# Performance work log

Hardware: AMD Instinct MI355X
Metric: run time of the kernel (lower is better)

Reference implementation:

```python
import jax, jax.numpy as jnp
import numpy as np

HEADS = 8
D = 1024


def setup_inputs() -> dict:
    key = jax.random.key(0)
    ks = jax.random.split(key, 10)
    B, Sq, Sk = 8, 2048, 2048
    x = jax.random.normal(ks[0], (B, Sq, D), dtype=jnp.float32)
    context = jax.random.normal(ks[1], (B, Sk, D), dtype=jnp.float32)
    # Dense params (glorot-ish scale)
    def dense(k, fin, fout):
        return jax.random.normal(k, (fin, fout), dtype=jnp.float32) / np.sqrt(fin)
    Wq = dense(ks[2], D, HEADS); bq = jnp.zeros((HEADS,), jnp.float32)
    Wk = dense(ks[3], D, HEADS); bk = jnp.zeros((HEADS,), jnp.float32)
    Wv = dense(ks[4], D, HEADS); bv = jnp.zeros((HEADS,), jnp.float32)
    Wo = dense(ks[5], HEADS, D); bo = jnp.zeros((D,), jnp.float32)
    return {"x": x, "context": context, "Wq": Wq, "bq": bq,
            "Wk": Wk, "bk": bk, "Wv": Wv, "bv": bv, "Wo": Wo, "bo": bo}


def reference(x, context, Wq, bq, Wk, bk, Wv, bv, Wo, bo):
    # q: [B,Sq,H], k/v: [B,Sk,H]  (H = heads = projection width, no head split)
    q = jnp.einsum('bsd,dh->bsh', x, Wq) + bq
    k = jnp.einsum('btd,dh->bth', context, Wk) + bk
    v = jnp.einsum('btd,dh->bth', context, Wv) + bv
    # Dot(axes=-1): scores[b,s,t] = q[b,s,:] . k[b,t,:]  -> [B,Sq,Sk]
    scores = jnp.einsum('bsh,bth->bst', q, k)
    weights = jax.nn.softmax(scores, axis=-1)  # no 1/sqrt(d) scaling in original
    # Dot(axes=(-1,1)): out[b,s,h] = sum_t weights[b,s,t] * v[b,t,h]
    out = jnp.einsum('bst,bth->bsh', weights, v)
    return jnp.einsum('bsh,hd->bsd', out, Wo) + bo
```

## Files before the change

### kernel.cpp

```cpp
#include <hip/hip_runtime.h>

constexpr int D = 1024;
constexpr int H = 8;
constexpr int S = 2048;
constexpr int B = 8;
constexpr int NROW = B * S;

__device__ __forceinline__ int swz(int i) { return i ^ ((i >> 3) & 7); }

__global__ __launch_bounds__(256)
void proj_kernel(const float* __restrict__ x, const float* __restrict__ ctx,
                 const float* __restrict__ Wq, const float* __restrict__ bq,
                 const float* __restrict__ Wk, const float* __restrict__ bk,
                 const float* __restrict__ Wv, const float* __restrict__ bv,
                 float* __restrict__ qo, float* __restrict__ ko,
                 float* __restrict__ vo)
{
    __shared__ float4 wlds[2048];
    const int tid = threadIdx.x;
    const int tensor = (int)blockIdx.x % 3;
    const int blk    = (int)blockIdx.x / 3;

    const float* W    = (tensor == 0) ? Wq : (tensor == 1) ? Wk : Wv;
    const float* bias = (tensor == 0) ? bq : (tensor == 1) ? bk : bv;
    const float* src  = (tensor == 0) ? x  : ctx;
    float*       dst  = (tensor == 0) ? qo : (tensor == 1) ? ko : vo;

    {
        const float4* w4 = (const float4*)W;
        for (int i = tid; i < 2048; i += 256) wlds[swz(i)] = w4[i];
    }
    __syncthreads();

    const int c    = tid & 15;
    const int team = tid >> 4;
    const int row0 = blk * 64 + team * 4;
    const float4* r0 = (const float4*)(src + (size_t)row0 * D);

    float4 a0[4], a1[4];
#pragma unroll
    for (int r = 0; r < 4; ++r) {
        a0[r] = make_float4(0.f, 0.f, 0.f, 0.f);
        a1[r] = make_float4(0.f, 0.f, 0.f, 0.f);
    }

#pragma unroll 2
    for (int j = 0; j < 16; ++j) {
        float4 xv[4];
#pragma unroll
        for (int r = 0; r < 4; ++r) xv[r] = r0[r * 256 + 16 * j + c];
        const int ib = 128 * j + 8 * c;
#pragma unroll
        for (int e = 0; e < 4; ++e) {
            const float4 w0 = wlds[swz(ib + 2 * e)];
            const float4 w1 = wlds[swz(ib + 2 * e + 1)];
#pragma unroll
            for (int r = 0; r < 4; ++r) {
                const float s = (&xv[r].x)[e];
                a0[r].x += s * w0.x; a0[r].y += s * w0.y;
                a0[r].z += s * w0.z; a0[r].w += s * w0.w;
                a1[r].x += s * w1.x; a1[r].y += s * w1.y;
                a1[r].z += s * w1.z; a1[r].w += s * w1.w;
            }
        }
    }

#pragma unroll
    for (int r = 0; r < 4; ++r) {
        float s[8] = {a0[r].x, a0[r].y, a0[r].z, a0[r].w,
                      a1[r].x, a1[r].y, a1[r].z, a1[r].w};
#pragma unroll
        for (int h = 0; h < 8; ++h) {
            s[h] += __shfl_down(s[h], 8);
            s[h] += __shfl_down(s[h], 4);
            s[h] += __shfl_down(s[h], 2);
            s[h] += __shfl_down(s[h], 1);
        }
        if (c == 0) {
            float4* o = (float4*)(dst + (size_t)(row0 + r) * H);
            o[0] = make_float4(s[0] + bias[0], s[1] + bias[1],
                               s[2] + bias[2], s[3] + bias[3]);
            o[1] = make_float4(s[4] + bias[4], s[5] + bias[5],
                               s[6] + bias[6], s[7] + bias[7]);
        }
    }
}

constexpr int ROWS_PER_WAVE = 4;
constexpr int ROWS_PER_BLOCK = 16;
constexpr int TILE_T = 512;

__global__ __launch_bounds__(256)
void attn_kernel(const float* __restrict__ q, const float* __restrict__ k,
                 const float* __restrict__ v, const float* __restrict__ Wo,
                 const float* __restrict__ bo, float* __restrict__ out)
{
    __shared__ float4 kt[TILE_T * 2];
    __shared__ float4 vt[TILE_T * 2];
    const int tid  = threadIdx.x;
    const int lane = tid & 63;
    const int wid  = tid >> 6;

    const int row0 = blockIdx.x * ROWS_PER_BLOCK + wid * ROWS_PER_WAVE;
    const int b = row0 >> 11;

    float qv[ROWS_PER_WAVE][H];
#pragma unroll
    for (int r = 0; r < ROWS_PER_WAVE; ++r) {
        const float4* q4 = (const float4*)(q + (size_t)(row0 + r) * H);
        const float4 a = q4[0], c = q4[1];
        qv[r][0] = a.x; qv[r][1] = a.y; qv[r][2] = a.z; qv[r][3] = a.w;
        qv[r][4] = c.x; qv[r][5] = c.y; qv[r][6] = c.z; qv[r][7] = c.w;
    }

    float l[ROWS_PER_WAVE] = {0.f, 0.f, 0.f, 0.f};
    float o[ROWS_PER_WAVE][H];
#pragma unroll
    for (int r = 0; r < ROWS_PER_WAVE; ++r)
#pragma unroll
        for (int h = 0; h < H; ++h) o[r][h] = 0.f;

    const float4* kg = (const float4*)(k + (size_t)b * S * H);
    const float4* vg = (const float4*)(v + (size_t)b * S * H);

    for (int tile = 0; tile < S / TILE_T; ++tile) {
        __syncthreads();
#pragma unroll
        for (int i = 0; i < 4; ++i) {
            kt[i * 256 + tid] = kg[tile * 1024 + i * 256 + tid];
            vt[i * 256 + tid] = vg[tile * 1024 + i * 256 + tid];
        }
        __syncthreads();
#pragma unroll 2
        for (int m = 0; m < TILE_T / 64; ++m) {
            const int t2 = (lane + (m << 6)) * 2;
            const float4 ka = kt[t2], kb = kt[t2 + 1];
            const float4 va = vt[t2], vb = vt[t2 + 1];
#pragma unroll
            for (int r = 0; r < ROWS_PER_WAVE; ++r) {
                const float s = qv[r][0] * ka.x + qv[r][1] * ka.y
                              + qv[r][2] * ka.z + qv[r][3] * ka.w
                              + qv[r][4] * kb.x + qv[r][5] * kb.y
                              + qv[r][6] * kb.z + qv[r][7] * kb.w;
                const float e = __expf(s);
                l[r] += e;
                o[r][0] += e * va.x; o[r][1] += e * va.y;
                o[r][2] += e * va.z; o[r][3] += e * va.w;
                o[r][4] += e * vb.x; o[r][5] += e * vb.y;
                o[r][6] += e * vb.z; o[r][7] += e * vb.w;
            }
        }
    }

#pragma unroll
    for (int r = 0; r < ROWS_PER_WAVE; ++r) {
#pragma unroll
        for (int off = 32; off > 0; off >>= 1) l[r] += __shfl_xor(l[r], off);
        const float inv = 1.f / l[r];
#pragma unroll
        for (int h = 0; h < H; ++h) {
#pragma unroll
            for (int off = 32; off > 0; off >>= 1) o[r][h] += __shfl_xor(o[r][h], off);
            o[r][h] *= inv;
        }
    }

    const float4* Wo4 = (const float4*)Wo;
    const float4* bo4 = (const float4*)bo;
    float4* out4 = (float4*)out;
#pragma unroll
    for (int c = 0; c < 4; ++c) {
        const int f = lane + 64 * c;
        float4 w[H];
#pragma unroll
        for (int h = 0; h < H; ++h) w[h] = Wo4[h * (D / 4) + f];
        const float4 base = bo4[f];
#pragma unroll
        for (int r = 0; r < ROWS_PER_WAVE; ++r) {
            float4 acc = base;
#pragma unroll
            for (int h = 0; h < H; ++h) {
                acc.x += o[r][h] * w[h].x;
                acc.y += o[r][h] * w[h].y;
                acc.z += o[r][h] * w[h].z;
                acc.w += o[r][h] * w[h].w;
            }
            out4[(size_t)(row0 + r) * (D / 4) + f] = acc;
        }
    }
}

extern "C" void kernel_launch(void* const* d_in, const int* in_sizes, int n_in,
                              void* d_out, int out_size, void* d_ws, size_t ws_size,
                              hipStream_t stream) {
    const float* x   = (const float*)d_in[0];
    const float* ctx = (const float*)d_in[1];
    const float* Wq  = (const float*)d_in[2];
    const float* bq  = (const float*)d_in[3];
    const float* Wk  = (const float*)d_in[4];
    const float* bk  = (const float*)d_in[5];
    const float* Wv  = (const float*)d_in[6];
    const float* bv  = (const float*)d_in[7];
    const float* Wo  = (const float*)d_in[8];
    const float* bo  = (const float*)d_in[9];
    float* out = (float*)d_out;

    float* qw = (float*)d_ws;
    float* kw = qw + (size_t)NROW * H;
    float* vw = kw + (size_t)NROW * H;

    proj_kernel<<<dim3(3 * NROW / 64), dim3(256), 0, stream>>>(
        x, ctx, Wq, bq, Wk, bk, Wv, bv, qw, kw, vw);
    attn_kernel<<<dim3(NROW / ROWS_PER_BLOCK), dim3(256), 0, stream>>>(
        qw, kw, vw, Wo, bo, out);
}
```

Baseline: 238.1 us.

## Prefetch x rows in projection, split K/V LDS tiles, double rows per wave

The projection kernel now keeps four register buffers of input rows and issues loads four steps ahead, so global-load latency overlaps the FMA work. The attention kernel doubles the query rows per wave (4→8, block 16→32 rows), reusing each K/V tile read from LDS across more rows and halving the number of times K/V are staged. K/V are also split into separate low/high float4 LDS arrays to avoid strided 32-byte LDS accesses. The cost is more registers per thread, which may lower occupancy, and half as many attention blocks.

```diff
diff --git a/kernel.cpp b/kernel.cpp
--- a/kernel.cpp
+++ b/kernel.cpp
@@ -44,11 +44,20 @@
         a1[r] = make_float4(0.f, 0.f, 0.f, 0.f);
     }
 
-#pragma unroll 2
-    for (int j = 0; j < 16; ++j) {
-        float4 xv[4];
-#pragma unroll
-        for (int r = 0; r < 4; ++r) xv[r] = r0[r * 256 + 16 * j + c];
+    float4 bA[4], bB[4], bC[4], bD[4];
+#pragma unroll
+    for (int r = 0; r < 4; ++r) {
+        bA[r] = r0[r * 256 +  0 + c];
+        bB[r] = r0[r * 256 + 16 + c];
+        bC[r] = r0[r * 256 + 32 + c];
+        bD[r] = r0[r * 256 + 48 + c];
+    }
+
+    auto step = [&](float4 (&buf)[4], int j) {
+        const int jp = (j + 4 < 16) ? j + 4 : 0;
+        float4 nxt[4];
+#pragma unroll
+        for (int r = 0; r < 4; ++r) nxt[r] = r0[r * 256 + 16 * jp + c];
         const int ib = 128 * j + 8 * c;
 #pragma unroll
         for (int e = 0; e < 4; ++e) {
@@ -56,13 +65,23 @@
             const float4 w1 = wlds[swz(ib + 2 * e + 1)];
 #pragma unroll
             for (int r = 0; r < 4; ++r) {
-                const float s = (&xv[r].x)[e];
+                const float s = (&buf[r].x)[e];
                 a0[r].x += s * w0.x; a0[r].y += s * w0.y;
                 a0[r].z += s * w0.z; a0[r].w += s * w0.w;
                 a1[r].x += s * w1.x; a1[r].y += s * w1.y;
                 a1[r].z += s * w1.z; a1[r].w += s * w1.w;
             }
         }
+#pragma unroll
+        for (int r = 0; r < 4; ++r) buf[r] = nxt[r];
+    };
+
+#pragma unroll
+    for (int j = 0; j < 16; j += 4) {
+        step(bA, j);
+        step(bB, j + 1);
+        step(bC, j + 2);
+        step(bD, j + 3);
     }
 
 #pragma unroll
@@ -86,8 +105,8 @@
     }
 }
 
-constexpr int ROWS_PER_WAVE = 4;
-constexpr int ROWS_PER_BLOCK = 16;
+constexpr int RPW = 8;
+constexpr int RPB = 32;
 constexpr int TILE_T = 512;
 
 __global__ __launch_bounds__(256)
@@ -95,30 +114,32 @@
                  const float* __restrict__ v, const float* __restrict__ Wo,
                  const float* __restrict__ bo, float* __restrict__ out)
 {
-    __shared__ float4 kt[TILE_T * 2];
-    __shared__ float4 vt[TILE_T * 2];
+    __shared__ float4 ka[TILE_T], kb[TILE_T];
+    __shared__ float4 va[TILE_T], vb[TILE_T];
     const int tid  = threadIdx.x;
     const int lane = tid & 63;
     const int wid  = tid >> 6;
 
-    const int row0 = blockIdx.x * ROWS_PER_BLOCK + wid * ROWS_PER_WAVE;
+    const int row0 = blockIdx.x * RPB + wid * RPW;
     const int b = row0 >> 11;
 
-    float qv[ROWS_PER_WAVE][H];
-#pragma unroll
-    for (int r = 0; r < ROWS_PER_WAVE; ++r) {
+    float qv[RPW][H];
+#pragma unroll
+    for (int r = 0; r < RPW; ++r) {
         const float4* q4 = (const float4*)(q + (size_t)(row0 + r) * H);
         const float4 a = q4[0], c = q4[1];
         qv[r][0] = a.x; qv[r][1] = a.y; qv[r][2] = a.z; qv[r][3] = a.w;
         qv[r][4] = c.x; qv[r][5] = c.y; qv[r][6] = c.z; qv[r][7] = c.w;
     }
 
-    float l[ROWS_PER_WAVE] = {0.f, 0.f, 0.f, 0.f};
-    float o[ROWS_PER_WAVE][H];
-#pragma unroll
-    for (int r = 0; r < ROWS_PER_WAVE; ++r)
+    float l[RPW];
+    float o[RPW][H];
+#pragma unroll
+    for (int r = 0; r < RPW; ++r) {
+        l[r] = 0.f;
 #pragma unroll
         for (int h = 0; h < H; ++h) o[r][h] = 0.f;
+    }
 
     const float4* kg = (const float4*)(k + (size_t)b * S * H);
     const float4* vg = (const float4*)(v + (size_t)b * S * H);
@@ -126,34 +147,36 @@
     for (int tile = 0; tile < S / TILE_T; ++tile) {
         __syncthreads();
 #pragma unroll
-        for (int i = 0; i < 4; ++i) {
-            kt[i * 256 + tid] = kg[tile * 1024 + i * 256 + tid];
-            vt[i * 256 + tid] = vg[tile * 1024 + i * 256 + tid];
+        for (int i = 0; i < TILE_T / 256; ++i) {
+            const int t = i * 256 + tid;
+            const int g = tile * TILE_T + t;
+            ka[t] = kg[2 * g];  kb[t] = kg[2 * g + 1];
+            va[t] = vg[2 * g];  vb[t] = vg[2 * g + 1];
         }
         __syncthreads();
 #pragma unroll 2
         for (int m = 0; m < TILE_T / 64; ++m) {
-            const int t2 = (lane + (m << 6)) * 2;
-            const float4 ka = kt[t2], kb = kt[t2 + 1];
-            const float4 va = vt[t2], vb = vt[t2 + 1];
-#pragma unroll
-            for (int r = 0; r < ROWS_PER_WAVE; ++r) {
-                const float s = qv[r][0] * ka.x + qv[r][1] * ka.y
-                              + qv[r][2] * ka.z + qv[r][3] * ka.w
-                              + qv[r][4] * kb.x + qv[r][5] * kb.y
-                              + qv[r][6] * kb.z + qv[r][7] * kb.w;
+            const int t = lane + (m << 6);
+            const float4 k0 = ka[t], k1 = kb[t];
+            const float4 v0 = va[t], v1 = vb[t];
+#pragma unroll
+            for (int r = 0; r < RPW; ++r) {
+                const float s = qv[r][0] * k0.x + qv[r][1] * k0.y
+                              + qv[r][2] * k0.z + qv[r][3] * k0.w
+                              + qv[r][4] * k1.x + qv[r][5] * k1.y
+                              + qv[r][6] * k1.z + qv[r][7] * k1.w;
                 const float e = __expf(s);
                 l[r] += e;
-                o[r][0] += e * va.x; o[r][1] += e * va.y;
-                o[r][2] += e * va.z; o[r][3] += e * va.w;
-                o[r][4] += e * vb.x; o[r][5] += e * vb.y;
-                o[r][6] += e * vb.z; o[r][7] += e * vb.w;
+                o[r][0] += e * v0.x; o[r][1] += e * v0.y;
+                o[r][2] += e * v0.z; o[r][3] += e * v0.w;
+                o[r][4] += e * v1.x; o[r][5] += e * v1.y;
+                o[r][6] += e * v1.z; o[r][7] += e * v1.w;
             }
         }
     }
 
 #pragma unroll
-    for (int r = 0; r < ROWS_PER_WAVE; ++r) {
+    for (int r = 0; r < RPW; ++r) {
 #pragma unroll
         for (int off = 32; off > 0; off >>= 1) l[r] += __shfl_xor(l[r], off);
         const float inv = 1.f / l[r];
@@ -176,7 +199,7 @@
         for (int h = 0; h < H; ++h) w[h] = Wo4[h * (D / 4) + f];
         const float4 base = bo4[f];
 #pragma unroll
-        for (int r = 0; r < ROWS_PER_WAVE; ++r) {
+        for (int r = 0; r < RPW; ++r) {
             float4 acc = base;
 #pragma unroll
             for (int h = 0; h < H; ++h) {
@@ -211,6 +234,6 @@
 
     proj_kernel<<<dim3(3 * NROW / 64), dim3(256), 0, stream>>>(
         x, ctx, Wq, bq, Wk, bk, Wv, bv, qw, kw, vw);
-    attn_kernel<<<dim3(NROW / ROWS_PER_BLOCK), dim3(256), 0, stream>>>(
+    attn_kernel<<<dim3(NROW / RPB), dim3(256), 0, stream>>>(
         qw, kw, vw, Wo, bo, out);
 }
```

After: 412.3 us. 73.1% more time.
